# Kernel optimization log

Hardware: AMD Instinct MI355X
Metric: run time of the kernel (lower is better)

Reference implementation:

```python
import jax, jax.numpy as jnp
import numpy as np
from jax import lax

WINDOW_SIZE = 11
SIGMA = 1.5
VAL_RANGE = 1000.0 / 10.0  # L = 100.0


def _gaussian_window(window_size, sigma, channel):
    # matches torch: exp(-(x - ws//2)^2 / (2*sigma^2)), normalized
    x = np.arange(window_size, dtype=np.float32)
    g = np.exp(-((x - window_size // 2) ** 2) / (2.0 * sigma ** 2))
    g = g / g.sum()
    w2d = np.outer(g, g).astype(np.float32)  # [ws, ws]
    # depthwise kernel, OIHW with I=1, O=channel
    w = np.broadcast_to(w2d, (channel, 1, window_size, window_size))
    return jnp.asarray(np.ascontiguousarray(w))


def _depthwise_conv(x, window, channel):
    # x: [B, C, H, W], window: [C, 1, ws, ws], valid padding, groups=C
    return lax.conv_general_dilated(
        x, window,
        window_strides=(1, 1), padding='VALID',
        dimension_numbers=('NCHW', 'OIHW', 'NCHW'),
        feature_group_count=channel)


def setup_inputs() -> dict:
    key = jax.random.key(0)
    k1, k2 = jax.random.split(key)
    B, C, H, W = 32, 1, 480, 640
    img1 = jax.random.uniform(k1, (B, C, H, W), dtype=jnp.float32)
    img2 = jax.random.uniform(k2, (B, C, H, W), dtype=jnp.float32)
    return {"img1": img1, "img2": img2}


def reference(img1, img2):
    channel = img1.shape[1]
    window = _gaussian_window(WINDOW_SIZE, SIGMA, channel)

    L = VAL_RANGE
    C1 = (0.01 * L) ** 2
    C2 = (0.03 * L) ** 2

    mu1 = _depthwise_conv(img1, window, channel)
    mu2 = _depthwise_conv(img2, window, channel)
    mu1_sq = mu1 * mu1
    mu2_sq = mu2 * mu2
    mu1_mu2 = mu1 * mu2

    sigma1_sq = _depthwise_conv(img1 * img1, window, channel) - mu1_sq
    sigma2_sq = _depthwise_conv(img2 * img2, window, channel) - mu2_sq
    sigma12 = _depthwise_conv(img1 * img2, window, channel) - mu1_mu2

    v1 = 2.0 * sigma12 + C2
    v2 = sigma1_sq + sigma2_sq + C2
    ssim_map = (2.0 * mu1_mu2 + C1) * v1 / ((mu1_sq + mu2_sq + C1) * v2)

    ret = jnp.mean(ssim_map)  # size_average=True
    L_ssim = (1.0 - ret) / 2.0
    return L_ssim
```

## Files before the change

### kernel.cpp

```cpp
#include <hip/hip_runtime.h>

#define IMG_H 480
#define IMG_W 640
#define OUT_H 470
#define OUT_W 630
#define NBATCH 32
#define SW 126
#define NSTRIPE 5
#define RCH 34
#define NCHUNK 14
#define WPB 2
#define NROWS (RCH + 10)

#define SSIM_C1 1.0f
#define SSIM_C2 9.0f

typedef float v2f __attribute__((ext_vector_type(2)));

__device__ constexpr float WG[11] = {
    0.00102838f, 0.00759876f, 0.03600077f, 0.10936068f, 0.21300554f,
    0.26601173f,
    0.21300554f, 0.10936068f, 0.03600077f, 0.00759876f, 0.00102838f
};

__device__ __forceinline__ v2f pk_fma(v2f a, v2f b, v2f c) {
    return __builtin_elementwise_fma(a, b, c);
}

#define STEP(IT, PP)                                                          \
  {                                                                           \
    const int P   = (PP) % 11;                                                \
    const int cur = (PP) & 1;                                                 \
    const int nxt = ((PP) + 1) & 1;                                           \
     \
    {                                                                         \
      int gy = y0 + (IT) + 1; if (gy > IMG_H - 1) gy = IMG_H - 1;             \
      const float* __restrict__ r1 = p1 + gy * IMG_W + colA;                  \
      const float* __restrict__ r2 = p2 + gy * IMG_W + colA;                  \
      _Pragma("unroll")                                                       \
      for (int k = 0; k < 6; ++k) {                                           \
        pb[nxt][0][k] = *(const v2f*)(r1 + 2 * k);                            \
        pb[nxt][1][k] = *(const v2f*)(r2 + 2 * k);                            \
      }                                                                       \
    }                                                                         \
            \
    v2f h1  = (v2f){0.f,0.f}, h2  = (v2f){0.f,0.f};                           \
    v2f h11 = (v2f){0.f,0.f}, h22 = (v2f){0.f,0.f}, h12 = (v2f){0.f,0.f};     \
    _Pragma("unroll")                                                         \
    for (int j = 0; j < 11; ++j) {                                            \
      const v2f wj = (v2f){WG[j], WG[j]};                                     \
      v2f q1, q2;                                                             \
      if (j & 1) {                                                            \
        q1 = (v2f){pb[cur][0][j >> 1].y, pb[cur][0][(j >> 1) + 1].x};         \
        q2 = (v2f){pb[cur][1][j >> 1].y, pb[cur][1][(j >> 1) + 1].x};         \
      } else {                                                                \
        q1 = pb[cur][0][j >> 1];                                              \
        q2 = pb[cur][1][j >> 1];                                              \
      }                                                                       \
      const v2f t1 = wj * q1;                                                 \
      const v2f t2 = wj * q2;                                                 \
      h1 += t1; h2 += t2;                                                     \
      h11 = pk_fma(t1, q1, h11);                                              \
      h22 = pk_fma(t2, q2, h22);                                              \
      h12 = pk_fma(t1, q2, h12);                                              \
    }                                                                         \
                              \
    _Pragma("unroll")                                                         \
    for (int sl = 0; sl < 11; ++sl) {                                         \
      const float wt = WG[(P - sl + 11) % 11];                                \
      const v2f wv = (v2f){wt, wt};                                           \
      acc[sl][0] = pk_fma(wv, h1,  acc[sl][0]);                               \
      acc[sl][1] = pk_fma(wv, h2,  acc[sl][1]);                               \
      acc[sl][2] = pk_fma(wv, h11, acc[sl][2]);                               \
      acc[sl][3] = pk_fma(wv, h22, acc[sl][3]);                               \
      acc[sl][4] = pk_fma(wv, h12, acc[sl][4]);                               \
    }                                                                         \
          \
    const int sc = (P + 1) % 11;                                              \
    if ((IT) >= 10 && (y0 + (IT) - 10) < OUT_H) {                             \
      const v2f m1 = acc[sc][0], m2 = acc[sc][1];                             \
      const v2f msq1 = m1 * m1, msq2 = m2 * m2, mu12 = m1 * m2;               \
      const v2f two = (v2f){2.f, 2.f};                                        \
      const v2f c1v = (v2f){SSIM_C1, SSIM_C1};                                \
      const v2f c2v = (v2f){SSIM_C2, SSIM_C2};                                \
      const v2f vA = pk_fma(two, acc[sc][4] - mu12, c2v);                     \
      const v2f vB = (acc[sc][2] - msq1) + (acc[sc][3] - msq2) + c2v;         \
      const v2f num = pk_fma(two, mu12, c1v) * vA;                            \
      const v2f den = (msq1 + msq2 + c1v) * vB;                               \
      if (validA) lsum = fmaf(num.x, __builtin_amdgcn_rcpf(den.x), lsum);     \
      if (validB) lsum = fmaf(num.y, __builtin_amdgcn_rcpf(den.y), lsum);     \
    }                                                                         \
    _Pragma("unroll")                                                         \
    for (int ch = 0; ch < 5; ++ch) acc[sc][ch] = (v2f){0.f, 0.f};             \
  }

__global__ __launch_bounds__(64 * WPB, 2) void ssim_main(
    const float* __restrict__ img1,
    const float* __restrict__ img2,
    float* __restrict__ partials)
{
    const int lane   = threadIdx.x & 63;
    const int wv     = threadIdx.x >> 6;
    const int stripe = blockIdx.x;
    const int cy     = blockIdx.y * WPB + wv;
    const int b      = blockIdx.z;
    const int x0 = SW * stripe;
    const int y0 = RCH * cy;

    const float* __restrict__ p1 = img1 + (size_t)b * (IMG_H * IMG_W);
    const float* __restrict__ p2 = img2 + (size_t)b * (IMG_H * IMG_W);

    int colA = x0 + 2 * lane;
    if (colA > IMG_W - 12) colA = IMG_W - 12;

    const bool validA = (2 * lane     < SW) && (x0 + 2 * lane     < OUT_W);
    const bool validB = (2 * lane + 1 < SW) && (x0 + 2 * lane + 1 < OUT_W);

    v2f acc[11][5];
#pragma unroll
    for (int i = 0; i < 11; ++i)
#pragma unroll
        for (int ch = 0; ch < 5; ++ch) acc[i][ch] = (v2f){0.f, 0.f};

    float lsum = 0.f;

    v2f pb[2][2][6];

    {
        const float* __restrict__ r1 = p1 + y0 * IMG_W + colA;
        const float* __restrict__ r2 = p2 + y0 * IMG_W + colA;
#pragma unroll
        for (int k = 0; k < 6; ++k) {
            pb[0][0][k] = *(const v2f*)(r1 + 2 * k);
            pb[0][1][k] = *(const v2f*)(r2 + 2 * k);
        }
    }

#pragma unroll 1
    for (int blk = 0; blk < 2; ++blk) {
        const int base = 22 * blk;
#pragma unroll
        for (int p = 0; p < 22; ++p) STEP(base + p, p)
    }

#pragma unroll
    for (int off = 32; off > 0; off >>= 1)
        lsum += __shfl_down(lsum, off);
    if (lane == 0)
        partials[(b * NCHUNK + cy) * NSTRIPE + stripe] = lsum;
}

__global__ __launch_bounds__(256) void ssim_reduce(
    const float* __restrict__ partials, float* __restrict__ out)
{
    const int n = NSTRIPE * NCHUNK * NBATCH;
    __shared__ double red[256];
    int tid = threadIdx.x;
    double s = 0.0;
    for (int i = tid; i < n; i += 256) s += (double)partials[i];
    red[tid] = s;
    __syncthreads();
    for (int k = 128; k > 0; k >>= 1) {
        if (tid < k) red[tid] += red[tid + k];
        __syncthreads();
    }
    if (tid == 0) {
        double mean = red[0] / (double)((size_t)NBATCH * OUT_H * OUT_W);
        out[0] = (float)((1.0 - mean) * 0.5);
    }
}

extern "C" void kernel_launch(void* const* d_in, const int* in_sizes, int n_in,
                              void* d_out, int out_size, void* d_ws, size_t ws_size,
                              hipStream_t stream)
{
    const float* img1 = (const float*)d_in[0];
    const float* img2 = (const float*)d_in[1];
    float* out = (float*)d_out;
    float* partials = (float*)d_ws;

    dim3 grid(NSTRIPE, NCHUNK / WPB, NBATCH);
    ssim_main<<<grid, dim3(64 * WPB), 0, stream>>>(img1, img2, partials);
    ssim_reduce<<<1, dim3(256), 0, stream>>>(partials, out);
}
```

Measured before the change: 135.4 us.

## Stream image rows into LDS via async global_load_lds with three-row prefetch

Replaces the per-lane register double-buffered row loads with direct global-to-LDS async loads (global_load_lds). Rows are staged into an 11-slot per-wave LDS ring three rows ahead, gated by an explicit vmcnt wait. The 44-step loop is also fully unrolled. The goal is deeper prefetch and coalesced dword loads that hide memory latency without holding row data in VGPRs. In exchange it adds LDS traffic and LDS reads per step, and a hand-written waitcnt. That waitcnt may be fragile, because no LDS visibility fence is issued before the reads of the staged data.

Result: slower. 141.2 us (+4.3%).

```diff
diff --git a/kernel.cpp b/kernel.cpp
--- a/kernel.cpp
+++ b/kernel.cpp
@@ -12,6 +12,10 @@
 #define WPB 2
 #define NROWS (RCH + 10)
 
+#define ROW_F  192
+#define SLOT_F 384
+#define NSLOT  11
+
 #define SSIM_C1 1.0f
 #define SSIM_C2 9.0f
 
@@ -27,23 +31,36 @@
     return __builtin_elementwise_fma(a, b, c);
 }
 
+#define GLL(gsrc, ldst)                                                       \
+  __builtin_amdgcn_global_load_lds(                                           \
+      (const __attribute__((address_space(1))) void*)(gsrc),                  \
+      (__attribute__((address_space(3))) void*)(ldst), 4, 0, 0)
+
 #define STEP(IT, PP)                                                          \
   {                                                                           \
-    const int P   = (PP) % 11;                                                \
-    const int cur = (PP) & 1;                                                 \
-    const int nxt = ((PP) + 1) & 1;                                           \
-     \
+    const int P   = (PP) % 11;                   \
+    const int wsl = ((PP) + 3) % 11;             \
+            \
     {                                                                         \
-      int gy = y0 + (IT) + 1; if (gy > IMG_H - 1) gy = IMG_H - 1;             \
-      const float* __restrict__ r1 = p1 + gy * IMG_W + colA;                  \
-      const float* __restrict__ r2 = p2 + gy * IMG_W + colA;                  \
+      int gy = y0 + (IT) + 3; if (gy > IMG_H - 1) gy = IMG_H - 1;             \
+      const float* r1 = p1 + gy * IMG_W;                                      \
+      const float* r2 = p2 + gy * IMG_W;                                      \
       _Pragma("unroll")                                                       \
-      for (int k = 0; k < 6; ++k) {                                           \
-        pb[nxt][0][k] = *(const v2f*)(r1 + 2 * k);                            \
-        pb[nxt][1][k] = *(const v2f*)(r2 + 2 * k);                            \
+      for (int i = 0; i < 3; ++i) {                                           \
+        GLL(r1 + coff[i], &swave[wsl * SLOT_F +         i * 64]);             \
+        GLL(r2 + coff[i], &swave[wsl * SLOT_F + ROW_F + i * 64]);             \
       }                                                                       \
     }                                                                         \
-            \
+              \
+    asm volatile("s_waitcnt vmcnt(18)" ::: "memory");                         \
+         \
+    v2f pb[2][6];                                                             \
+    _Pragma("unroll")                                                         \
+    for (int k = 0; k < 6; ++k) {                                             \
+      pb[0][k] = *(const v2f*)&swave[P * SLOT_F +         2 * lane + 2 * k];  \
+      pb[1][k] = *(const v2f*)&swave[P * SLOT_F + ROW_F + 2 * lane + 2 * k];  \
+    }                                                                         \
+                      \
     v2f h1  = (v2f){0.f,0.f}, h2  = (v2f){0.f,0.f};                           \
     v2f h11 = (v2f){0.f,0.f}, h22 = (v2f){0.f,0.f}, h12 = (v2f){0.f,0.f};     \
     _Pragma("unroll")                                                         \
@@ -51,11 +68,11 @@
       const v2f wj = (v2f){WG[j], WG[j]};                                     \
       v2f q1, q2;                                                             \
       if (j & 1) {                                                            \
-        q1 = (v2f){pb[cur][0][j >> 1].y, pb[cur][0][(j >> 1) + 1].x};         \
-        q2 = (v2f){pb[cur][1][j >> 1].y, pb[cur][1][(j >> 1) + 1].x};         \
+        q1 = (v2f){pb[0][j >> 1].y, pb[0][(j >> 1) + 1].x};                   \
+        q2 = (v2f){pb[1][j >> 1].y, pb[1][(j >> 1) + 1].x};                   \
       } else {                                                                \
-        q1 = pb[cur][0][j >> 1];                                              \
-        q2 = pb[cur][1][j >> 1];                                              \
+        q1 = pb[0][j >> 1];                                                   \
+        q2 = pb[1][j >> 1];                                                   \
       }                                                                       \
       const v2f t1 = wj * q1;                                                 \
       const v2f t2 = wj * q2;                                                 \
@@ -68,12 +85,12 @@
     _Pragma("unroll")                                                         \
     for (int sl = 0; sl < 11; ++sl) {                                         \
       const float wt = WG[(P - sl + 11) % 11];                                \
-      const v2f wv = (v2f){wt, wt};                                           \
-      acc[sl][0] = pk_fma(wv, h1,  acc[sl][0]);                               \
-      acc[sl][1] = pk_fma(wv, h2,  acc[sl][1]);                               \
-      acc[sl][2] = pk_fma(wv, h11, acc[sl][2]);                               \
-      acc[sl][3] = pk_fma(wv, h22, acc[sl][3]);                               \
-      acc[sl][4] = pk_fma(wv, h12, acc[sl][4]);                               \
+      const v2f wv2 = (v2f){wt, wt};                                          \
+      acc[sl][0] = pk_fma(wv2, h1,  acc[sl][0]);                              \
+      acc[sl][1] = pk_fma(wv2, h2,  acc[sl][1]);                              \
+      acc[sl][2] = pk_fma(wv2, h11, acc[sl][2]);                              \
+      acc[sl][3] = pk_fma(wv2, h22, acc[sl][3]);                              \
+      acc[sl][4] = pk_fma(wv2, h12, acc[sl][4]);                              \
     }                                                                         \
           \
     const int sc = (P + 1) % 11;                                              \
@@ -110,8 +127,13 @@
     const float* __restrict__ p1 = img1 + (size_t)b * (IMG_H * IMG_W);
     const float* __restrict__ p2 = img2 + (size_t)b * (IMG_H * IMG_W);
 
-    int colA = x0 + 2 * lane;
-    if (colA > IMG_W - 12) colA = IMG_W - 12;
+    __shared__ __align__(16) float sbuf[WPB][NSLOT * SLOT_F];
+    float* swave = &sbuf[wv][0];
+
+    int coff[3];
+    coff[0] = x0 + lane;
+    coff[1] = x0 + 64 + lane;
+    coff[2] = x0 + 128 + lane; if (coff[2] > IMG_W - 1) coff[2] = IMG_W - 1;
 
     const bool validA = (2 * lane     < SW) && (x0 + 2 * lane     < OUT_W);
     const bool validB = (2 * lane + 1 < SW) && (x0 + 2 * lane + 1 < OUT_W);
@@ -124,24 +146,21 @@
 
     float lsum = 0.f;
 
-    v2f pb[2][2][6];
-
-    {
-        const float* __restrict__ r1 = p1 + y0 * IMG_W + colA;
-        const float* __restrict__ r2 = p2 + y0 * IMG_W + colA;
-#pragma unroll
-        for (int k = 0; k < 6; ++k) {
-            pb[0][0][k] = *(const v2f*)(r1 + 2 * k);
-            pb[0][1][k] = *(const v2f*)(r2 + 2 * k);
+#pragma unroll
+    for (int r = 0; r < 3; ++r) {
+        const float* r1 = p1 + (y0 + r) * IMG_W;
+        const float* r2 = p2 + (y0 + r) * IMG_W;
+#pragma unroll
+        for (int i = 0; i < 3; ++i) {
+            GLL(r1 + coff[i], &swave[r * SLOT_F +         i * 64]);
+            GLL(r2 + coff[i], &swave[r * SLOT_F + ROW_F + i * 64]);
         }
     }
 
-#pragma unroll 1
-    for (int blk = 0; blk < 2; ++blk) {
-        const int base = 22 * blk;
-#pragma unroll
-        for (int p = 0; p < 22; ++p) STEP(base + p, p)
-    }
+#pragma unroll
+    for (int p = 0; p < 44; ++p) STEP(p, p)
+
+    asm volatile("s_waitcnt vmcnt(0)" ::: "memory");
 
 #pragma unroll
     for (int off = 32; off > 0; off >>= 1)
```
